# Optimization experiments

Measured on AMD Instinct MI355X. Metric: run time of the kernel, lower is better.

## Reference

```python
import jax, jax.numpy as jnp
import numpy as np

OUT_F = 8192
IN_F = 8192
B, T = 1, 16
ZERO_POINT = 128.0  # center the simulated fp8/int codes


def setup_inputs() -> dict:
    key = jax.random.key(0)
    k_x, k_w, k_s, k_b = jax.random.split(key, 4)
    x = jax.random.normal(k_x, (B, T, IN_F), dtype=jnp.float32)
    # simulated low-precision weight codes (stands in for fp8_data)
    w_q = jax.random.randint(k_w, (OUT_F, IN_F), 0, 256, dtype=jnp.int32)
    # per-output-channel dequant scale (small positive values)
    scale = jax.random.uniform(k_s, (OUT_F,), dtype=jnp.float32) * 0.01 + 1e-4
    bias = jax.random.normal(k_b, (OUT_F,), dtype=jnp.float32)
    return {"x": x, "w_q": w_q, "scale": scale, "bias": bias}


def reference(x, w_q, scale, bias):
    # dequantize: codes -> float, per-row scale (materializes full-precision W,
    # as the original module does before F.linear)
    w = (w_q.astype(jnp.float32) - ZERO_POINT) * scale[:, None]  # [out, in]
    # F.linear: x @ W^T + b
    out = jnp.einsum('bti,oi->bto', x, w) + bias
    return out
```

## Files before the change

kernel.cpp:

```cpp
#include <hip/hip_runtime.h>


#define IN_F   8192
#define OUT_F  8192
#define NT     16
#define BLOCK  256
#define W_O    2
#define CH_PER_BLOCK 8
#define K_CHUNK 256
#define NCHUNK (IN_F / K_CHUNK)

typedef float f32x2 __attribute__((ext_vector_type(2)));

__global__ __launch_bounds__(BLOCK, 2)
void qlin_kernel(const float* __restrict__ x,
                 const int*   __restrict__ w_q,
                 const float* __restrict__ scale,
                 const float* __restrict__ bias,
                 float* __restrict__ out)
{
    __shared__ float xs[2][NT][K_CHUNK];

    const int tid  = threadIdx.x;
    const int lane = tid & 63;
    const int wave = tid >> 6;
    const int o_base = blockIdx.x * CH_PER_BLOCK + wave * W_O;

    const int* __restrict__ wr0 = w_q + (size_t)(o_base + 0) * IN_F;
    const int* __restrict__ wr1 = w_q + (size_t)(o_base + 1) * IN_F;

#define STAGE(c, b)                                                          \
    {                                                                        \
        _Pragma("unroll")                                                    \
        for (int r = 0; r < 4; ++r) {                                        \
            const int row = r * 4 + wave;                                    \
            const char* g = (const char*)x + (size_t)row * (IN_F * 4) +      \
                            (size_t)(c) * 1024 + lane * 16;                  \
            char* l = (char*)(&xs[0][0][0]) + (b) * 16384 + row * 1024;      \
            __builtin_amdgcn_global_load_lds(                                \
                (const __attribute__((address_space(1))) void*)g,            \
                (__attribute__((address_space(3))) void*)l, 16, 0, 0);       \
        }                                                                    \
    }

#define WPF(WA, WB, c)                                                       \
    WA = *reinterpret_cast<const int4*>(wr0 + (c) * K_CHUNK + lane * 4);     \
    WB = *reinterpret_cast<const int4*>(wr1 + (c) * K_CHUNK + lane * 4);

#define FMA(WA, WB, cur)                                                     \
    {                                                                        \
        f32x2 wf[4];                                                         \
        wf[0] = (f32x2){(float)(WA.x - 128), (float)(WB.x - 128)};           \
        wf[1] = (f32x2){(float)(WA.y - 128), (float)(WB.y - 128)};           \
        wf[2] = (f32x2){(float)(WA.z - 128), (float)(WB.z - 128)};           \
        wf[3] = (f32x2){(float)(WA.w - 128), (float)(WB.w - 128)};           \
        _Pragma("unroll")                                                    \
        for (int t = 0; t < NT; ++t) {                                       \
            const float4 xv = *reinterpret_cast<const float4*>(              \
                &xs[cur][t][lane * 4]);                                      \
            acc2[t] += wf[0] * (f32x2){xv.x, xv.x};                          \
            acc2[t] += wf[1] * (f32x2){xv.y, xv.y};                          \
            acc2[t] += wf[2] * (f32x2){xv.z, xv.z};                          \
            acc2[t] += wf[3] * (f32x2){xv.w, xv.w};                          \
        }                                                                    \
    }

#define CHUNK(c, WA_CUR, WB_CUR, WA_NXT, WB_NXT)                             \
    {                                                                        \
        if ((c) + 1 < NCHUNK) {                                              \
            STAGE((c) + 1, ((c) & 1) ^ 1)                                    \
            __builtin_amdgcn_sched_barrier(0);                               \
            WPF(WA_NXT, WB_NXT, (c) + 1)                                     \
        }                                                                    \
        __builtin_amdgcn_sched_barrier(0);                                   \
        FMA(WA_CUR, WB_CUR, (c) & 1)                                         \
        __builtin_amdgcn_sched_barrier(0);                                   \
        if ((c) + 1 < NCHUNK) {                                              \
            asm volatile("s_waitcnt vmcnt(2) lgkmcnt(0)" ::: "memory");      \
            __builtin_amdgcn_s_barrier();                                    \
            __builtin_amdgcn_sched_barrier(0);                               \
        }                                                                    \
    }

    f32x2 acc2[NT];
#pragma unroll
    for (int t = 0; t < NT; ++t) acc2[t] = (f32x2)0.0f;

    int4 a0, a1, b0, b1;

    STAGE(0, 0)
    __builtin_amdgcn_sched_barrier(0);
    WPF(a0, a1, 0)
    __builtin_amdgcn_sched_barrier(0);
    asm volatile("s_waitcnt vmcnt(2)" ::: "memory");
    __builtin_amdgcn_s_barrier();
    __builtin_amdgcn_sched_barrier(0);

#pragma unroll 1
    for (int cc = 0; cc < NCHUNK; cc += 2) {
        CHUNK(cc + 0, a0, a1, b0, b1)
        CHUNK(cc + 1, b0, b1, a0, a1)
    }

#undef STAGE
#undef WPF
#undef FMA
#undef CHUNK

    float myval = 0.0f;
#pragma unroll
    for (int t = 0; t < NT; ++t) {
#pragma unroll
        for (int j = 0; j < W_O; ++j) {
            float v = acc2[t][j];
#pragma unroll
            for (int off = 32; off > 0; off >>= 1)
                v += __shfl_xor(v, off, 64);
            if (lane == (t * W_O + j)) myval = v;
        }
    }

    if (lane < NT * W_O) {
        const int t_o = lane >> 1;
        const int o   = o_base + (lane & 1);
        out[(size_t)t_o * OUT_F + o] = myval * scale[o] + bias[o];
    }
}

extern "C" void kernel_launch(void* const* d_in, const int* in_sizes, int n_in,
                              void* d_out, int out_size, void* d_ws, size_t ws_size,
                              hipStream_t stream) {
    const float* x     = (const float*)d_in[0];
    const int*   w_q   = (const int*)d_in[1];
    const float* scale = (const float*)d_in[2];
    const float* bias  = (const float*)d_in[3];
    float*       out   = (float*)d_out;

    dim3 grid(OUT_F / CH_PER_BLOCK);
    dim3 block(BLOCK);
    qlin_kernel<<<grid, block, 0, stream>>>(x, w_q, scale, bias, out);
}
```

Before: 78.29 us.

## Halve K chunk and use four-buffer LDS ring with prefetch distance two

Shrinks the K chunk from 256 to 128 and replaces the x double buffer with a four-slot LDS ring, so x staging runs two chunks ahead of compute. Weight prefetch stays one chunk ahead but each lane now loads int2 instead of int4. The per-chunk vmcnt wait is removed; completion of the staged x data now relies on the compiler's implicit wait for the weight registers, which were issued after it. The aim is to hide x-staging latency better, at the cost of fewer bytes in flight per weight load and twice as many barriers.

Measured after the change: 67.58 us. 13.7% less time.

```diff
diff --git a/kernel.cpp b/kernel.cpp
--- a/kernel.cpp
+++ b/kernel.cpp
@@ -7,8 +7,9 @@
 #define BLOCK  256
 #define W_O    2
 #define CH_PER_BLOCK 8
-#define K_CHUNK 256
+#define K_CHUNK 128
 #define NCHUNK (IN_F / K_CHUNK)
+#define NBUF   4
 
 typedef float f32x2 __attribute__((ext_vector_type(2)));
 
@@ -19,7 +20,7 @@
                  const float* __restrict__ bias,
                  float* __restrict__ out)
 {
-    __shared__ float xs[2][NT][K_CHUNK];
+    __shared__ float xs[NBUF][NT][K_CHUNK];
 
     const int tid  = threadIdx.x;
     const int lane = tid & 63;
@@ -32,11 +33,13 @@
 #define STAGE(c, b)                                                          \
     {                                                                        \
         _Pragma("unroll")                                                    \
-        for (int r = 0; r < 4; ++r) {                                        \
-            const int row = r * 4 + wave;                                    \
+        for (int i = 0; i < 2; ++i) {                                        \
+            const int seg = wave * 2 + i;                                    \
+            const int row = seg * 2 + (lane >> 5);                           \
             const char* g = (const char*)x + (size_t)row * (IN_F * 4) +      \
-                            (size_t)(c) * 1024 + lane * 16;                  \
-            char* l = (char*)(&xs[0][0][0]) + (b) * 16384 + row * 1024;      \
+                            (size_t)(c) * (K_CHUNK * 4) + (lane & 31) * 16;  \
+            char* l = (char*)(&xs[0][0][0]) + (b) * (NT * K_CHUNK * 4) +     \
+                      seg * 1024;                                            \
             __builtin_amdgcn_global_load_lds(                                \
                 (const __attribute__((address_space(1))) void*)g,            \
                 (__attribute__((address_space(3))) void*)l, 16, 0, 0);       \
@@ -44,39 +47,32 @@
     }
 
 #define WPF(WA, WB, c)                                                       \
-    WA = *reinterpret_cast<const int4*>(wr0 + (c) * K_CHUNK + lane * 4);     \
-    WB = *reinterpret_cast<const int4*>(wr1 + (c) * K_CHUNK + lane * 4);
+    WA = *reinterpret_cast<const int2*>(wr0 + (c) * K_CHUNK + lane * 2);     \
+    WB = *reinterpret_cast<const int2*>(wr1 + (c) * K_CHUNK + lane * 2);
 
-#define FMA(WA, WB, cur)                                                     \
+#define FMA(WA, WB, b)                                                       \
     {                                                                        \
-        f32x2 wf[4];                                                         \
-        wf[0] = (f32x2){(float)(WA.x - 128), (float)(WB.x - 128)};           \
-        wf[1] = (f32x2){(float)(WA.y - 128), (float)(WB.y - 128)};           \
-        wf[2] = (f32x2){(float)(WA.z - 128), (float)(WB.z - 128)};           \
-        wf[3] = (f32x2){(float)(WA.w - 128), (float)(WB.w - 128)};           \
+        const f32x2 wf0 = (f32x2){(float)(WA.x - 128), (float)(WB.x - 128)}; \
+        const f32x2 wf1 = (f32x2){(float)(WA.y - 128), (float)(WB.y - 128)}; \
         _Pragma("unroll")                                                    \
         for (int t = 0; t < NT; ++t) {                                       \
-            const float4 xv = *reinterpret_cast<const float4*>(              \
-                &xs[cur][t][lane * 4]);                                      \
-            acc2[t] += wf[0] * (f32x2){xv.x, xv.x};                          \
-            acc2[t] += wf[1] * (f32x2){xv.y, xv.y};                          \
-            acc2[t] += wf[2] * (f32x2){xv.z, xv.z};                          \
-            acc2[t] += wf[3] * (f32x2){xv.w, xv.w};                          \
+            const float2 xv = *reinterpret_cast<const float2*>(              \
+                &xs[b][t][lane * 2]);                                        \
+            acc2[t] += wf0 * (f32x2){xv.x, xv.x};                            \
+            acc2[t] += wf1 * (f32x2){xv.y, xv.y};                            \
         }                                                                    \
     }
 
 #define CHUNK(c, WA_CUR, WB_CUR, WA_NXT, WB_NXT)                             \
     {                                                                        \
-        if ((c) + 1 < NCHUNK) {                                              \
-            STAGE((c) + 1, ((c) & 1) ^ 1)                                    \
-            __builtin_amdgcn_sched_barrier(0);                               \
-            WPF(WA_NXT, WB_NXT, (c) + 1)                                     \
-        }                                                                    \
+        if ((c) + 2 < NCHUNK) STAGE((c) + 2, ((c) + 2) & 3)                  \
         __builtin_amdgcn_sched_barrier(0);                                   \
-        FMA(WA_CUR, WB_CUR, (c) & 1)                                         \
+        if ((c) + 1 < NCHUNK) { WPF(WA_NXT, WB_NXT, (c) + 1) }               \
+        __builtin_amdgcn_sched_barrier(0);                                   \
+        FMA(WA_CUR, WB_CUR, (c) & 3)                                         \
         __builtin_amdgcn_sched_barrier(0);                                   \
         if ((c) + 1 < NCHUNK) {                                              \
-            asm volatile("s_waitcnt vmcnt(2) lgkmcnt(0)" ::: "memory");      \
+            asm volatile("s_waitcnt lgkmcnt(0)" ::: "memory");               \
             __builtin_amdgcn_s_barrier();                                    \
             __builtin_amdgcn_sched_barrier(0);                               \
         }                                                                    \
@@ -86,13 +82,15 @@
 #pragma unroll
     for (int t = 0; t < NT; ++t) acc2[t] = (f32x2)0.0f;
 
-    int4 a0, a1, b0, b1;
+    int2 a0, a1, b0, b1;
 
     STAGE(0, 0)
     __builtin_amdgcn_sched_barrier(0);
+    STAGE(1, 1)
+    __builtin_amdgcn_sched_barrier(0);
     WPF(a0, a1, 0)
     __builtin_amdgcn_sched_barrier(0);
-    asm volatile("s_waitcnt vmcnt(2)" ::: "memory");
+    asm volatile("s_waitcnt vmcnt(4)" ::: "memory");
     __builtin_amdgcn_s_barrier();
     __builtin_amdgcn_sched_barrier(0);
 
```
